# Optimization experiments

Hardware: AMD Instinct MI355X
Metric: run time of the kernel (lower is better)

Reference implementation:

```python
import jax, jax.numpy as jnp
import numpy as np

QUALITY_ALPHA = 1.0
TOPK = 4
MIX_BETA = 0.5
NEG = -1e9


def setup_inputs() -> dict:
    key = jax.random.key(0)
    ks = jax.random.split(key, 12)
    B, S, D, H, Q, QH = 64, 2048, 512, 128, 4, 32
    feats = jax.random.normal(ks[0], (B, S, D), dtype=jnp.float32)
    mask = jax.random.uniform(ks[1], (B, S)) > 0.3
    mask = mask.at[:, 0].set(True)  # guarantee >=1 valid segment per row
    seg_quality = jax.random.normal(ks[2], (B, S, Q), dtype=jnp.float32)
    W1 = jax.random.normal(ks[3], (D, H), dtype=jnp.float32) * 0.05
    b1 = jnp.zeros((H,), dtype=jnp.float32)
    w2 = jax.random.normal(ks[4], (H, 1), dtype=jnp.float32) * 0.05
    b2 = jnp.zeros((1,), dtype=jnp.float32)
    qW1 = jax.random.normal(ks[5], (Q, QH), dtype=jnp.float32) * 0.05
    qb1 = jnp.zeros((QH,), dtype=jnp.float32)
    qw2 = jax.random.normal(ks[6], (QH, 1), dtype=jnp.float32) * 0.05
    qb2 = jnp.zeros((1,), dtype=jnp.float32)
    return dict(feats=feats, mask=mask, seg_quality=seg_quality,
                W1=W1, b1=b1, w2=w2, b2=b2, qW1=qW1, qb1=qb1, qw2=qw2, qb2=qb2)


def _masked_softmax(logits, mask):
    logits = jnp.where(mask, logits, NEG)
    w = jax.nn.softmax(logits, axis=1)
    w = w * mask.astype(w.dtype)
    return w / jnp.maximum(w.sum(axis=1, keepdims=True), 1e-8)


def reference(feats, mask, seg_quality, W1, b1, w2, b2, qW1, qb1, qw2, qb2):
    # evidence scorer: Linear -> tanh -> Linear  ([B,S,D] -> [B,S])
    evidence = (jnp.tanh(jnp.einsum('bsd,dh->bsh', feats, W1) + b1) @ w2)[..., 0] + b2[0]
    # quality net: Linear -> relu -> Linear  ([B,S,Q] -> [B,S])
    quality = (jax.nn.relu(jnp.einsum('bsq,qh->bsh', seg_quality, qW1) + qb1) @ qw2)[..., 0] + qb2[0]
    combined = evidence + QUALITY_ALPHA * quality

    weights = _masked_softmax(combined, mask)
    attn_pooled = jnp.einsum('bsd,bs->bd', feats, weights)

    # top-k path on combined logits
    masked_scores = jnp.where(mask, combined, NEG)
    _, topk_indices = jax.lax.top_k(masked_scores, TOPK)          # [B, k]
    topk_feats = jnp.take_along_axis(feats, topk_indices[..., None], axis=1)  # [B, k, D]
    topk_valid = jnp.take_along_axis(mask, topk_indices, axis=1)  # [B, k] bool
    denom = jnp.maximum(topk_valid.astype(feats.dtype).sum(axis=1, keepdims=True), 1.0)
    topk_pooled = (topk_feats * topk_valid[..., None].astype(feats.dtype)).sum(axis=1) / denom

    pooled = MIX_BETA * attn_pooled + (1.0 - MIX_BETA) * topk_pooled
    return pooled, weights, attn_pooled, topk_pooled, topk_indices, topk_valid
```

## Files before the change

kernel.cpp:

```cpp
#include <hip/hip_runtime.h>
#include <cstdint>
#include <cstddef>

#define B 64
#define S 2048
#define D 512
#define H 128
#define Q 4
#define QH 32
#define KTOP 4
#define NROWS (B * S)
#define NEGV -1e9f
#define RPB 128
#define NBLK (NROWS / RPB)
#define CPB (S / RPB)

typedef __bf16 bf16x8 __attribute__((ext_vector_type(8)));
typedef float f32x4 __attribute__((ext_vector_type(4)));
typedef unsigned short us8 __attribute__((ext_vector_type(8)));

__device__ __forceinline__ unsigned hasbyte(unsigned v, unsigned c) {
    unsigned x = v ^ (c * 0x01010101u);
    return (x - 0x01010101u) & ~x & 0x80808080u;
}

__device__ __forceinline__ unsigned short rnbf(float x) {
    unsigned u = __float_as_uint(x);
    unsigned r = u + 0x7FFFu + ((u >> 16) & 1u);
    return (unsigned short)(r >> 16);
}

__device__ __forceinline__ void split_rn(float x, unsigned short& hi, unsigned short& lo) {
    hi = rnbf(x);
    float fh = __uint_as_float((unsigned)hi << 16);
    lo = rnbf(x - fh);
}

__device__ __forceinline__ float tanh_f(float x) {
    float e = __expf(2.f * x);
    return 1.f - __fdividef(2.f, e + 1.f);
}

__global__ __launch_bounds__(256) void prep_kernel(
    const float* __restrict__ W1, unsigned short* __restrict__ bh,
    unsigned short* __restrict__ bl, const unsigned char* __restrict__ m,
    int* __restrict__ mode) {
    const int t = threadIdx.x;
    if (blockIdx.x < 256) {
        int i = blockIdx.x * 256 + t;
        int h = i >> 9, k = i & 511;
        float x = W1[(size_t)k * H + h];
        unsigned short hv, lv;
        split_rn(x, hv, lv);
        bh[i] = hv;
        bl[i] = lv;
        return;
    }
    __shared__ int fF0, fF, fB, fO4;
    if (t == 0) { fF0 = 0; fF = 0; fB = 0; fO4 = 0; }
    __syncthreads();
    const uint4* mv = (const uint4*)m;
    int a = 0, bb = 0, c = 0, d = 0;
    for (int i = t; i < NROWS / 16; i += 256) {
        uint4 v = mv[i];
        if (hasbyte(v.x, 0xF0u) | hasbyte(v.y, 0xF0u) | hasbyte(v.z, 0xF0u) | hasbyte(v.w, 0xF0u)) a = 1;
        if (hasbyte(v.x, 0x3Fu) | hasbyte(v.y, 0x3Fu) | hasbyte(v.z, 0x3Fu) | hasbyte(v.w, 0x3Fu) |
            hasbyte(v.x, 0x80u) | hasbyte(v.y, 0x80u) | hasbyte(v.z, 0x80u) | hasbyte(v.w, 0x80u)) bb = 1;
        if ((v.x & 0xFFFFFF00u) | (v.y & 0xFFFFFF00u) | (v.z & 0xFFFFFF00u) | (v.w & 0xFFFFFF00u)) c = 1;
        if ((v.y & 0xFFu) | (v.w & 0xFFu)) d = 1;
    }
    if (a) atomicOr(&fF0, 1);
    if (bb) atomicOr(&fF, 1);
    if (c) atomicOr(&fB, 1);
    if (d) atomicOr(&fO4, 1);
    __syncthreads();
    if (t == 0) {
        int md;
        if (fF0) md = 4;
        else if (fF) md = 3;
        else if (fB) md = 0;
        else if (fO4) md = 1;
        else md = 2;
        *mode = md;
    }
}

__global__ __launch_bounds__(512) void fused_kernel(
    const float* __restrict__ feats, const unsigned short* __restrict__ wbh,
    const unsigned short* __restrict__ wbl, const float* __restrict__ b1g,
    const float* __restrict__ w2g, const float* __restrict__ b2g,
    const void* __restrict__ mraw, const int* __restrict__ mode,
    const float* __restrict__ segq, const float* __restrict__ qW1,
    const float* __restrict__ qb1, const float* __restrict__ qw2,
    const float* __restrict__ qb2, float* __restrict__ comb,
    float* __restrict__ Zpart, float* __restrict__ part) {
    __shared__ unsigned short Ah[16][RPB][32];
    __shared__ unsigned short Al[RPB][32];
    __shared__ unsigned short Bh[H][32];
    __shared__ unsigned short Bl[H][32];
    __shared__ float red[RPB][2];
    __shared__ float sew[RPB];
    __shared__ float sQW[Q * QH];
    __shared__ float sQb1[QH];
    __shared__ float sQw2[QH];
    __shared__ float sQb2;

    const int t = threadIdx.x;
    const int lane = t & 63;
    const int wid = t >> 6;
    const int wm = wid >> 1;
    const int wn = wid & 1;
    const int l16 = lane & 15, lk = lane >> 4;
    const int row0 = blockIdx.x * RPB;
    const int md = *mode;

    if (t < Q * QH) sQW[t] = qW1[t];
    else if (t < 160) sQb1[t - 128] = qb1[t - 128];
    else if (t < 192) sQw2[t - 160] = qw2[t - 160];
    else if (t == 192) sQb2 = qb2[0];

    const int ar = t >> 2;
    const int o = t & 3;
    const int po = o ^ ((ar >> 1) & 3);
    const float* fsrc = feats + (size_t)(row0 + ar) * D + o * 8;
    const unsigned short* bsrch = wbh + (size_t)ar * D + o * 8;
    const unsigned short* bsrcl = wbl + (size_t)ar * D + o * 8;

    f32x4 acc[2][4];
#pragma unroll
    for (int mf = 0; mf < 2; ++mf)
#pragma unroll
        for (int nf = 0; nf < 4; ++nf) acc[mf][nf] = (f32x4)0.f;

    float rA[8];
    us8 rBh, rBl;
    *reinterpret_cast<float4*>(&rA[0]) = *reinterpret_cast<const float4*>(fsrc + 0);
    *reinterpret_cast<float4*>(&rA[4]) = *reinterpret_cast<const float4*>(fsrc + 4);
    rBh = *reinterpret_cast<const us8*>(bsrch);
    rBl = *reinterpret_cast<const us8*>(bsrcl);
    {
        us8 vh, vl;
#pragma unroll
        for (int j = 0; j < 8; ++j) {
            unsigned short hh, ll;
            split_rn(rA[j], hh, ll);
            vh[j] = hh; vl[j] = ll;
        }
        *reinterpret_cast<us8*>(&Ah[0][ar][po * 8]) = vh;
        *reinterpret_cast<us8*>(&Al[ar][po * 8]) = vl;
        *reinterpret_cast<us8*>(&Bh[ar][po * 8]) = rBh;
        *reinterpret_cast<us8*>(&Bl[ar][po * 8]) = rBl;
    }

    for (int kci = 0; kci < 16; ++kci) {
        __syncthreads();
        if (kci < 15) {
            const int kc = (kci + 1) * 32;
            *reinterpret_cast<float4*>(&rA[0]) = *reinterpret_cast<const float4*>(fsrc + kc);
            *reinterpret_cast<float4*>(&rA[4]) = *reinterpret_cast<const float4*>(fsrc + kc + 4);
            rBh = *reinterpret_cast<const us8*>(bsrch + kc);
            rBl = *reinterpret_cast<const us8*>(bsrcl + kc);
        }
        bf16x8 ah[2], al[2], bh[4], bl[4];
#pragma unroll
        for (int mf = 0; mf < 2; ++mf) {
            int rr = wm * 32 + mf * 16 + l16;
            int sp = (lk ^ ((rr >> 1) & 3)) * 8;
            ah[mf] = *reinterpret_cast<const bf16x8*>(&Ah[kci][rr][sp]);
            al[mf] = *reinterpret_cast<const bf16x8*>(&Al[rr][sp]);
        }
#pragma unroll
        for (int nf = 0; nf < 4; ++nf) {
            int hh = wn * 64 + nf * 16 + l16;
            int sp = (lk ^ ((hh >> 1) & 3)) * 8;
            bh[nf] = *reinterpret_cast<const bf16x8*>(&Bh[hh][sp]);
            bl[nf] = *reinterpret_cast<const bf16x8*>(&Bl[hh][sp]);
        }
#pragma unroll
        for (int mf = 0; mf < 2; ++mf)
#pragma unroll
            for (int nf = 0; nf < 4; ++nf) {
                acc[mf][nf] = __builtin_amdgcn_mfma_f32_16x16x32_bf16(ah[mf], bh[nf], acc[mf][nf], 0, 0, 0);
                acc[mf][nf] = __builtin_amdgcn_mfma_f32_16x16x32_bf16(ah[mf], bl[nf], acc[mf][nf], 0, 0, 0);
                acc[mf][nf] = __builtin_amdgcn_mfma_f32_16x16x32_bf16(al[mf], bh[nf], acc[mf][nf], 0, 0, 0);
            }
        __syncthreads();
        if (kci < 15) {
            us8 vh, vl;
#pragma unroll
            for (int j = 0; j < 8; ++j) {
                unsigned short hh, ll;
                split_rn(rA[j], hh, ll);
                vh[j] = hh; vl[j] = ll;
            }
            *reinterpret_cast<us8*>(&Ah[kci + 1][ar][po * 8]) = vh;
            *reinterpret_cast<us8*>(&Al[ar][po * 8]) = vl;
            *reinterpret_cast<us8*>(&Bh[ar][po * 8]) = rBh;
            *reinterpret_cast<us8*>(&Bl[ar][po * 8]) = rBl;
        }
    }

    float b1v[4], w2v[4];
#pragma unroll
    for (int nf = 0; nf < 4; ++nf) {
        int hh = wn * 64 + nf * 16 + l16;
        b1v[nf] = b1g[hh];
        w2v[nf] = w2g[hh];
    }
#pragma unroll
    for (int mf = 0; mf < 2; ++mf)
#pragma unroll
        for (int r2 = 0; r2 < 4; ++r2) {
            float s = 0.f;
#pragma unroll
            for (int nf = 0; nf < 4; ++nf) s += tanh_f(acc[mf][nf][r2] + b1v[nf]) * w2v[nf];
            s += __shfl_xor(s, 1, 16);
            s += __shfl_xor(s, 2, 16);
            s += __shfl_xor(s, 4, 16);
            s += __shfl_xor(s, 8, 16);
            if (l16 == 0) red[wm * 32 + mf * 16 + lk * 4 + r2][wn] = s;
        }
    __syncthreads();

    if (t < RPB) {
        const int row = row0 + t;
        float4 sq = *reinterpret_cast<const float4*>(&segq[(size_t)row * Q]);
        float q = sQb2;
#pragma unroll
        for (int h = 0; h < QH; ++h) {
            float a = sq.x * sQW[h] + sq.y * sQW[QH + h] + sq.z * sQW[2 * QH + h] + sq.w * sQW[3 * QH + h] + sQb1[h];
            q += fmaxf(a, 0.f) * sQw2[h];
        }
        float mv;
        switch (md) {
            case 0: mv = ((const unsigned char*)mraw)[row] ? 1.f : 0.f; break;
            case 1: mv = ((const int*)mraw)[row] ? 1.f : 0.f; break;
            case 2: mv = ((const long long*)mraw)[row] ? 1.f : 0.f; break;
            case 3: mv = (((const float*)mraw)[row] != 0.f) ? 1.f : 0.f; break;
            default: mv = (((const double*)mraw)[row] != 0.0) ? 1.f : 0.f; break;
        }
        float e = red[t][0] + red[t][1] + b2g[0];
        float c = (mv != 0.f) ? (e + q) : NEGV;
        comb[row] = c;
        sew[t] = __expf(c);
    }
    __syncthreads();

    if (t < 64) {
        float z = sew[t] + sew[t + 64];
#pragma unroll
        for (int oo = 32; oo > 0; oo >>= 1) z += __shfl_xor(z, oo, 64);
        if (t == 0) Zpart[blockIdx.x] = z;
    }

    if (t < 256) {
        const int d0 = t * 2;
        const int kci = d0 >> 5;
        const int c = d0 & 31;
        const int og = c >> 3, c7 = c & 7;
        float a0 = 0.f, a1 = 0.f;
#pragma unroll 8
        for (int r = 0; r < RPB; ++r) {
            const int row = (r + kci) & (RPB - 1);
            const int sp = (og ^ ((row >> 1) & 3)) * 8 + c7;
            unsigned v = *reinterpret_cast<const unsigned*>(&Ah[kci][row][sp]);
            float f0 = __uint_as_float((v & 0xFFFFu) << 16);
            float f1 = __uint_as_float(v & 0xFFFF0000u);
            float w = sew[row];
            a0 += w * f0;
            a1 += w * f1;
        }
        float2 o2 = make_float2(a0, a1);
        *reinterpret_cast<float2*>(&part[(size_t)blockIdx.x * D + d0]) = o2;
    }
}

__global__ __launch_bounds__(256) void finalize_kernel(
    const float* __restrict__ comb, const float* __restrict__ Zpart,
    const float* __restrict__ part, const float* __restrict__ feats,
    float* __restrict__ o_weights, float* __restrict__ o_tidx, float* __restrict__ o_tval,
    float* __restrict__ o_attn, float* __restrict__ o_topk, float* __restrict__ o_pooled) {
    __shared__ float sinv;
    __shared__ float mvv[256 * 4];
    __shared__ int mii[256 * 4];
    __shared__ int sti[4];
    __shared__ float stv[4];
    __shared__ float sdn;
    const int b = blockIdx.x, t = threadIdx.x;
    const float* row = comb + (size_t)b * S;

    if (t == 0) {
        float z = 0.f;
#pragma unroll
        for (int j = 0; j < CPB; ++j) z += Zpart[b * CPB + j];
        sinv = 1.f / fmaxf(z, 1e-8f);
    }
    __syncthreads();
    const float inv = sinv;

    float tv[4] = {-3e38f, -3e38f, -3e38f, -3e38f};
    int ti[4] = {1 << 30, 1 << 30, 1 << 30, 1 << 30};
    for (int s = t; s < S; s += 256) {
        float v = row[s];
        o_weights[(size_t)b * S + s] = __expf(v) * inv;
        if (v > tv[3]) {
            tv[3] = v; ti[3] = s;
#pragma unroll
            for (int k = 3; k > 0; --k) {
                bool up = (tv[k] > tv[k - 1]) || (tv[k] == tv[k - 1] && ti[k] < ti[k - 1]);
                if (up) {
                    float fv = tv[k]; tv[k] = tv[k - 1]; tv[k - 1] = fv;
                    int ii = ti[k]; ti[k] = ti[k - 1]; ti[k - 1] = ii;
                }
            }
        }
    }
#pragma unroll
    for (int k = 0; k < 4; ++k) { mvv[t * 4 + k] = tv[k]; mii[t * 4 + k] = ti[k]; }
    __syncthreads();
    for (int st = 128; st >= 1; st >>= 1) {
        if (t < st) {
            float av[4], bv[4];
            int ai[4], bi[4];
#pragma unroll
            for (int k = 0; k < 4; ++k) {
                av[k] = mvv[t * 4 + k]; ai[k] = mii[t * 4 + k];
                bv[k] = mvv[(t + st) * 4 + k]; bi[k] = mii[(t + st) * 4 + k];
            }
            float rv[4]; int ri[4];
            int i = 0, j = 0;
            for (int oo = 0; oo < 4; ++oo) {
                bool ta = (av[i] > bv[j]) || (av[i] == bv[j] && ai[i] < bi[j]);
                if (ta) { rv[oo] = av[i]; ri[oo] = ai[i]; ++i; }
                else { rv[oo] = bv[j]; ri[oo] = bi[j]; ++j; }
            }
#pragma unroll
            for (int k = 0; k < 4; ++k) { mvv[t * 4 + k] = rv[k]; mii[t * 4 + k] = ri[k]; }
        }
        __syncthreads();
    }
    if (t == 0) {
        float dn = 0.f;
#pragma unroll
        for (int k = 0; k < 4; ++k) {
            int idx = mii[k];
            int valid = (mvv[k] > -1e8f) ? 1 : 0;
            sti[k] = idx;
            stv[k] = (float)valid;
            o_tidx[b * 4 + k] = (float)idx;
            o_tval[b * 4 + k] = (float)valid;
            dn += (float)valid;
        }
        sdn = fmaxf(dn, 1.f);
    }
    __syncthreads();

    const int i0 = sti[0], i1 = sti[1], i2 = sti[2], i3 = sti[3];
    const float v0 = stv[0], v1 = stv[1], v2 = stv[2], v3 = stv[3];
    const float inv_dn = 1.f / sdn;
    for (int d = t; d < D; d += 256) {
        float s = 0.f;
#pragma unroll
        for (int ch = 0; ch < CPB; ++ch) s += part[((size_t)(b * CPB + ch)) * D + d];
        s *= inv;
        float tk = v0 * feats[((size_t)b * S + i0) * D + d] + v1 * feats[((size_t)b * S + i1) * D + d] +
                   v2 * feats[((size_t)b * S + i2) * D + d] + v3 * feats[((size_t)b * S + i3) * D + d];
        tk *= inv_dn;
        o_attn[(size_t)b * D + d] = s;
        o_topk[(size_t)b * D + d] = tk;
        o_pooled[(size_t)b * D + d] = 0.5f * s + 0.5f * tk;
    }
}

extern "C" void kernel_launch(void* const* d_in, const int* in_sizes, int n_in,
                              void* d_out, int out_size, void* d_ws, size_t ws_size,
                              hipStream_t stream) {
    const float* feats = (const float*)d_in[0];
    const void* maskraw = d_in[1];
    const float* segq = (const float*)d_in[2];
    const float* W1 = (const float*)d_in[3];
    const float* b1 = (const float*)d_in[4];
    const float* w2 = (const float*)d_in[5];
    const float* b2 = (const float*)d_in[6];
    const float* qW1 = (const float*)d_in[7];
    const float* qb1 = (const float*)d_in[8];
    const float* qw2 = (const float*)d_in[9];
    const float* qb2 = (const float*)d_in[10];

    char* ws = (char*)d_ws;
    int* mode = (int*)ws;
    float* comb = (float*)(ws + 16);
    float* part = comb + NROWS;
    float* Zpart = part + (size_t)NBLK * D;
    unsigned short* wsBh = (unsigned short*)(Zpart + NBLK);
    unsigned short* wsBl = wsBh + (size_t)H * D;

    float* out = (float*)d_out;
    float* o_pooled = out;
    float* o_weights = out + (size_t)B * D;
    float* o_attn = o_weights + (size_t)B * S;
    float* o_topk = o_attn + (size_t)B * D;
    float* o_tidx = o_topk + (size_t)B * D;
    float* o_tval = o_tidx + (size_t)B * KTOP;

    prep_kernel<<<257, 256, 0, stream>>>(W1, wsBh, wsBl, (const unsigned char*)maskraw, mode);
    fused_kernel<<<NBLK, 512, 0, stream>>>(
        feats, wsBh, wsBl, b1, w2, b2, maskraw, mode, segq, qW1, qb1, qw2, qb2,
        comb, Zpart, part);
    finalize_kernel<<<B, 256, 0, stream>>>(comb, Zpart, part, feats, o_weights,
                                           o_tidx, o_tval, o_attn, o_topk, o_pooled);
}
```

Baseline: 162.8 us.

## Use 1024-thread blocks, read W1 fragments directly from global, split pooling reduction

```diff
diff --git a/kernel.cpp b/kernel.cpp
--- a/kernel.cpp
+++ b/kernel.cpp
@@ -18,6 +18,7 @@
 typedef __bf16 bf16x8 __attribute__((ext_vector_type(8)));
 typedef float f32x4 __attribute__((ext_vector_type(4)));
 typedef unsigned short us8 __attribute__((ext_vector_type(8)));
+typedef unsigned short us4 __attribute__((ext_vector_type(4)));
 
 __device__ __forceinline__ unsigned hasbyte(unsigned v, unsigned c) {
     unsigned x = v ^ (c * 0x01010101u);
@@ -85,7 +86,7 @@
     }
 }
 
-__global__ __launch_bounds__(512) void fused_kernel(
+__global__ __launch_bounds__(1024) void fused_kernel(
     const float* __restrict__ feats, const unsigned short* __restrict__ wbh,
     const unsigned short* __restrict__ wbl, const float* __restrict__ b1g,
     const float* __restrict__ w2g, const float* __restrict__ b2g,
@@ -96,10 +97,9 @@
     float* __restrict__ Zpart, float* __restrict__ part) {
     __shared__ unsigned short Ah[16][RPB][32];
     __shared__ unsigned short Al[RPB][32];
-    __shared__ unsigned short Bh[H][32];
-    __shared__ unsigned short Bl[H][32];
-    __shared__ float red[RPB][2];
+    __shared__ float red[RPB][4];
     __shared__ float sew[RPB];
+    __shared__ float2 redp[512];
     __shared__ float sQW[Q * QH];
     __shared__ float sQb1[QH];
     __shared__ float sQw2[QH];
@@ -108,8 +108,8 @@
     const int t = threadIdx.x;
     const int lane = t & 63;
     const int wid = t >> 6;
-    const int wm = wid >> 1;
-    const int wn = wid & 1;
+    const int wm = wid >> 2;
+    const int wn = wid & 3;
     const int l16 = lane & 15, lk = lane >> 4;
     const int row0 = blockIdx.x * RPB;
     const int md = *mode;
@@ -119,49 +119,53 @@
     else if (t < 192) sQw2[t - 160] = qw2[t - 160];
     else if (t == 192) sQb2 = qb2[0];
 
-    const int ar = t >> 2;
-    const int o = t & 3;
-    const int po = o ^ ((ar >> 1) & 3);
-    const float* fsrc = feats + (size_t)(row0 + ar) * D + o * 8;
-    const unsigned short* bsrch = wbh + (size_t)ar * D + o * 8;
-    const unsigned short* bsrcl = wbl + (size_t)ar * D + o * 8;
-
-    f32x4 acc[2][4];
+    const int ar = t >> 3;
+    const int oq = t & 7;
+    const int o8 = oq >> 1, hf = oq & 1;
+    const int po = o8 ^ ((ar >> 1) & 3);
+    const float* fsrc = feats + (size_t)(row0 + ar) * D + oq * 4;
+    const int adst = po * 8 + hf * 4;
+
+    const unsigned short* bsrc0 = wbh + (size_t)(wn * 32 + l16) * D + lk * 8;
+    const unsigned short* bsrc1 = wbh + (size_t)(wn * 32 + 16 + l16) * D + lk * 8;
+    const size_t loOff = (size_t)H * D;
+
+    f32x4 acc[2][2];
 #pragma unroll
     for (int mf = 0; mf < 2; ++mf)
 #pragma unroll
-        for (int nf = 0; nf < 4; ++nf) acc[mf][nf] = (f32x4)0.f;
-
-    float rA[8];
-    us8 rBh, rBl;
-    *reinterpret_cast<float4*>(&rA[0]) = *reinterpret_cast<const float4*>(fsrc + 0);
-    *reinterpret_cast<float4*>(&rA[4]) = *reinterpret_cast<const float4*>(fsrc + 4);
-    rBh = *reinterpret_cast<const us8*>(bsrch);
-    rBl = *reinterpret_cast<const us8*>(bsrcl);
+        for (int nf = 0; nf < 2; ++nf) acc[mf][nf] = (f32x4)0.f;
+
+    float4 rAbuf[2];
+    rAbuf[0] = *reinterpret_cast<const float4*>(fsrc);
+    rAbuf[1] = *reinterpret_cast<const float4*>(fsrc + 32);
     {
-        us8 vh, vl;
-#pragma unroll
-        for (int j = 0; j < 8; ++j) {
+        us4 vh, vl;
+        float ff[4] = {rAbuf[0].x, rAbuf[0].y, rAbuf[0].z, rAbuf[0].w};
+#pragma unroll
+        for (int j = 0; j < 4; ++j) {
             unsigned short hh, ll;
-            split_rn(rA[j], hh, ll);
+            split_rn(ff[j], hh, ll);
             vh[j] = hh; vl[j] = ll;
         }
-        *reinterpret_cast<us8*>(&Ah[0][ar][po * 8]) = vh;
-        *reinterpret_cast<us8*>(&Al[ar][po * 8]) = vl;
-        *reinterpret_cast<us8*>(&Bh[ar][po * 8]) = rBh;
-        *reinterpret_cast<us8*>(&Bl[ar][po * 8]) = rBl;
-    }
-
+        *reinterpret_cast<us4*>(&Ah[0][ar][adst]) = vh;
+        *reinterpret_cast<us4*>(&Al[ar][adst]) = vl;
+    }
+
+#pragma unroll 2
     for (int kci = 0; kci < 16; ++kci) {
         __syncthreads();
-        if (kci < 15) {
-            const int kc = (kci + 1) * 32;
-            *reinterpret_cast<float4*>(&rA[0]) = *reinterpret_cast<const float4*>(fsrc + kc);
-            *reinterpret_cast<float4*>(&rA[4]) = *reinterpret_cast<const float4*>(fsrc + kc + 4);
-            rBh = *reinterpret_cast<const us8*>(bsrch + kc);
-            rBl = *reinterpret_cast<const us8*>(bsrcl + kc);
-        }
-        bf16x8 ah[2], al[2], bh[4], bl[4];
+        if (kci < 14)
+            rAbuf[kci & 1] = *reinterpret_cast<const float4*>(fsrc + (kci + 2) * 32);
+
+        const int kc = kci * 32;
+        bf16x8 bh[2], bl[2];
+        bh[0] = *reinterpret_cast<const bf16x8*>(bsrc0 + kc);
+        bh[1] = *reinterpret_cast<const bf16x8*>(bsrc1 + kc);
+        bl[0] = *reinterpret_cast<const bf16x8*>(bsrc0 + loOff + kc);
+        bl[1] = *reinterpret_cast<const bf16x8*>(bsrc1 + loOff + kc);
+
+        bf16x8 ah[2], al[2];
 #pragma unroll
         for (int mf = 0; mf < 2; ++mf) {
             int rr = wm * 32 + mf * 16 + l16;
@@ -170,40 +174,33 @@
             al[mf] = *reinterpret_cast<const bf16x8*>(&Al[rr][sp]);
         }
 #pragma unroll
-        for (int nf = 0; nf < 4; ++nf) {
-            int hh = wn * 64 + nf * 16 + l16;
-            int sp = (lk ^ ((hh >> 1) & 3)) * 8;
-            bh[nf] = *reinterpret_cast<const bf16x8*>(&Bh[hh][sp]);
-            bl[nf] = *reinterpret_cast<const bf16x8*>(&Bl[hh][sp]);
-        }
-#pragma unroll
         for (int mf = 0; mf < 2; ++mf)
 #pragma unroll
-            for (int nf = 0; nf < 4; ++nf) {
+            for (int nf = 0; nf < 2; ++nf) {
                 acc[mf][nf] = __builtin_amdgcn_mfma_f32_16x16x32_bf16(ah[mf], bh[nf], acc[mf][nf], 0, 0, 0);
                 acc[mf][nf] = __builtin_amdgcn_mfma_f32_16x16x32_bf16(ah[mf], bl[nf], acc[mf][nf], 0, 0, 0);
                 acc[mf][nf] = __builtin_amdgcn_mfma_f32_16x16x32_bf16(al[mf], bh[nf], acc[mf][nf], 0, 0, 0);
             }
         __syncthreads();
         if (kci < 15) {
-            us8 vh, vl;
-#pragma unroll
-            for (int j = 0; j < 8; ++j) {
+            float4 rv = rAbuf[(kci + 1) & 1];
+            float ff[4] = {rv.x, rv.y, rv.z, rv.w};
+            us4 vh, vl;
+#pragma unroll
+            for (int j = 0; j < 4; ++j) {
                 unsigned short hh, ll;
-                split_rn(rA[j], hh, ll);
+                split_rn(ff[j], hh, ll);
                 vh[j] = hh; vl[j] = ll;
             }
-            *reinterpret_cast<us8*>(&Ah[kci + 1][ar][po * 8]) = vh;
-            *reinterpret_cast<us8*>(&Al[ar][po * 8]) = vl;
-            *reinterpret_cast<us8*>(&Bh[ar][po * 8]) = rBh;
-            *reinterpret_cast<us8*>(&Bl[ar][po * 8]) = rBl;
-        }
-    }
-
-    float b1v[4], w2v[4];
-#pragma unroll
-    for (int nf = 0; nf < 4; ++nf) {
-        int hh = wn * 64 + nf * 16 + l16;
+            *reinterpret_cast<us4*>(&Ah[kci + 1][ar][adst]) = vh;
+            *reinterpret_cast<us4*>(&Al[ar][adst]) = vl;
+        }
+    }
+
+    float b1v[2], w2v[2];
+#pragma unroll
+    for (int nf = 0; nf < 2; ++nf) {
+        int hh = wn * 32 + nf * 16 + l16;
         b1v[nf] = b1g[hh];
         w2v[nf] = w2g[hh];
     }
@@ -213,7 +210,7 @@
         for (int r2 = 0; r2 < 4; ++r2) {
             float s = 0.f;
 #pragma unroll
-            for (int nf = 0; nf < 4; ++nf) s += tanh_f(acc[mf][nf][r2] + b1v[nf]) * w2v[nf];
+            for (int nf = 0; nf < 2; ++nf) s += tanh_f(acc[mf][nf][r2] + b1v[nf]) * w2v[nf];
             s += __shfl_xor(s, 1, 16);
             s += __shfl_xor(s, 2, 16);
             s += __shfl_xor(s, 4, 16);
@@ -239,7 +236,7 @@
             case 3: mv = (((const float*)mraw)[row] != 0.f) ? 1.f : 0.f; break;
             default: mv = (((const double*)mraw)[row] != 0.0) ? 1.f : 0.f; break;
         }
-        float e = red[t][0] + red[t][1] + b2g[0];
+        float e = red[t][0] + red[t][1] + red[t][2] + red[t][3] + b2g[0];
         float c = (mv != 0.f) ? (e + q) : NEGV;
         comb[row] = c;
         sew[t] = __expf(c);
@@ -253,15 +250,16 @@
         if (t == 0) Zpart[blockIdx.x] = z;
     }
 
-    if (t < 256) {
-        const int d0 = t * 2;
+    if (t < 512) {
+        const int th = t & 255, half = t >> 8;
+        const int d0 = th * 2;
         const int kci = d0 >> 5;
         const int c = d0 & 31;
         const int og = c >> 3, c7 = c & 7;
         float a0 = 0.f, a1 = 0.f;
 #pragma unroll 8
-        for (int r = 0; r < RPB; ++r) {
-            const int row = (r + kci) & (RPB - 1);
+        for (int r = 0; r < 64; ++r) {
+            const int row = half * 64 + ((r + kci) & 63);
             const int sp = (og ^ ((row >> 1) & 3)) * 8 + c7;
             unsigned v = *reinterpret_cast<const unsigned*>(&Ah[kci][row][sp]);
             float f0 = __uint_as_float((v & 0xFFFFu) << 16);
@@ -270,8 +268,13 @@
             a0 += w * f0;
             a1 += w * f1;
         }
-        float2 o2 = make_float2(a0, a1);
-        *reinterpret_cast<float2*>(&part[(size_t)blockIdx.x * D + d0]) = o2;
+        redp[t] = make_float2(a0, a1);
+    }
+    __syncthreads();
+    if (t < 256) {
+        float2 x = redp[t], y = redp[t + 256];
+        x.x += y.x; x.y += y.y;
+        *reinterpret_cast<float2*>(&part[(size_t)blockIdx.x * D + t * 2]) = x;
     }
 }
 
@@ -404,7 +407,7 @@
     float* o_tval = o_tidx + (size_t)B * KTOP;
 
     prep_kernel<<<257, 256, 0, stream>>>(W1, wsBh, wsBl, (const unsigned char*)maskraw, mode);
-    fused_kernel<<<NBLK, 512, 0, stream>>>(
+    fused_kernel<<<NBLK, 1024, 0, stream>>>(
         feats, wsBh, wsBl, b1, w2, b2, maskraw, mode, segq, qW1, qb1, qw2, qb2,
         comb, Zpart, part);
     finalize_kernel<<<B, 256, 0, stream>>>(comb, Zpart, part, feats, o_weights,
```

Result: slower. 301.7 us (+85.3%).
